# Optimization experiments

Hardware: AMD Instinct MI355X
Metric: run time of the kernel (lower is better)

## Reference

```python
import jax, jax.numpy as jnp
import numpy as np


def _conv(x, w, stride=1, pad=0):
    return jax.lax.conv_general_dilated(
        x, w, window_strides=(stride, stride),
        padding=[(pad, pad), (pad, pad)],
        dimension_numbers=('NCHW', 'OIHW', 'NCHW'))


def _frozen_bn(x, gamma, beta, mean, var):
    # FrozenBatchNorm2d: scale = gamma * rsqrt(var); bias = beta - mean*scale
    scale = gamma * jax.lax.rsqrt(var)
    bias = beta - mean * scale
    return x * scale[None, :, None, None] + bias[None, :, None, None]


def setup_inputs() -> dict:
    key = jax.random.key(0)
    ks = jax.random.split(key, 16)
    N, Cin, H, W = 32, 1024, 28, 28
    Cb, Cout = 256, 1024
    x = jax.random.normal(ks[0], (N, Cin, H, W), dtype=jnp.float32)
    # conv weights, kaiming-uniform-ish scale
    w1 = jax.random.uniform(ks[1], (Cb, Cin, 1, 1), minval=-1, maxval=1) * (1.0 / np.sqrt(Cin))
    w2 = jax.random.uniform(ks[2], (Cb, Cb, 3, 3), minval=-1, maxval=1) * (1.0 / np.sqrt(Cb * 9))
    w3 = jax.random.uniform(ks[3], (Cout, Cb, 1, 1), minval=-1, maxval=1) * (1.0 / np.sqrt(Cb))
    def bn_params(k, n):
        k1, k2, k3, k4 = jax.random.split(k, 4)
        gamma = jax.random.uniform(k1, (n,), minval=0.5, maxval=1.5)
        beta = jax.random.normal(k2, (n,)) * 0.1
        mean = jax.random.normal(k3, (n,)) * 0.1
        var = jax.random.uniform(k4, (n,), minval=0.5, maxval=1.5)
        return gamma, beta, mean, var
    g1, b1, m1, v1 = bn_params(ks[4], Cb)
    g2, b2, m2, v2 = bn_params(ks[5], Cb)
    g3, b3, m3, v3 = bn_params(ks[6], Cout)
    return dict(x=x, w1=w1, w2=w2, w3=w3,
                g1=g1, b1=b1, m1=m1, v1=v1,
                g2=g2, b2=b2, m2=m2, v2=v2,
                g3=g3, b3=b3, m3=m3, v3=v3)


def reference(x, w1, w2, w3, g1, b1, m1, v1, g2, b2, m2, v2, g3, b3, m3, v3):
    identity = x
    out = _conv(x, w1, stride=1, pad=0)          # 1x1: Cin -> Cb
    out = jax.nn.relu(_frozen_bn(out, g1, b1, m1, v1))
    out = _conv(out, w2, stride=1, pad=1)        # 3x3: Cb -> Cb
    out = jax.nn.relu(_frozen_bn(out, g2, b2, m2, v2))
    out = _conv(out, w3, stride=1, pad=0)        # 1x1: Cb -> Cout
    out = _frozen_bn(out, g3, b3, m3, v3)
    # stride==1 and in_channels==out_channels -> downsample is None
    out = jax.nn.relu(out + identity)
    return out
```

## Files before the change

### kernel.cpp

```cpp
#include <hip/hip_runtime.h>


#define BM 128
#define BNT 128
#define BK 64

typedef __attribute__((ext_vector_type(8))) short short8;
typedef __attribute__((ext_vector_type(4))) float f32x4;

__device__ inline unsigned short f2bf(float f) {
    unsigned int u = __float_as_uint(f);
    u += 0x7fff + ((u >> 16) & 1);
    return (unsigned short)(u >> 16);
}

__device__ inline void gload16(const unsigned short* g, unsigned short* l) {
    __builtin_amdgcn_global_load_lds(
        (const __attribute__((address_space(1))) unsigned int*)g,
        (__attribute__((address_space(3))) unsigned int*)l, 16, 0, 0);
}

__global__ __launch_bounds__(256) void prep_x(const float* __restrict__ x,
                                              unsigned short* __restrict__ Xh) {
    __shared__ float t[32][33];
    const int p0 = blockIdx.x * 32, c0 = blockIdx.y * 32, n = blockIdx.z;
    const int tid = threadIdx.x;
    const int pl = tid & 31, cl = tid >> 5;
    const float* xb = x + ((size_t)n * 1024 + c0) * 784;
    #pragma unroll
    for (int j = 0; j < 4; ++j) {
        int ci = cl + j * 8;
        int p = p0 + pl;
        t[ci][pl] = (p < 784) ? xb[(size_t)ci * 784 + p] : 0.f;
    }
    __syncthreads();
    const int c2 = (tid & 15) * 2, pr = tid >> 4;
    #pragma unroll
    for (int j = 0; j < 2; ++j) {
        int p = p0 + pr + j * 16;
        if (p < 784) {
            unsigned int pk = (unsigned)f2bf(t[c2][pr + j * 16]) |
                              ((unsigned)f2bf(t[c2 + 1][pr + j * 16]) << 16);
            *(unsigned int*)(Xh + (size_t)(n * 784 + p) * 1024 + c0 + c2) = pk;
        }
    }
}

__global__ __launch_bounds__(256) void prep_w(
    const float* __restrict__ w1, const float* __restrict__ w2, const float* __restrict__ w3,
    const float* g1, const float* b1, const float* m1, const float* v1,
    const float* g2, const float* b2, const float* m2, const float* v2,
    const float* g3, const float* b3, const float* m3, const float* v3,
    unsigned short* __restrict__ Wb1, unsigned short* __restrict__ Wt2,
    unsigned short* __restrict__ Wb3,
    float* __restrict__ bn1, float* __restrict__ bn2, float* __restrict__ bn3) {
    int i = blockIdx.x * 256 + threadIdx.x;
    if (i < 262144) Wb1[i] = f2bf(w1[i]);
    if (i < 589824) {
        int kw = i % 3, t1 = i / 3;
        int kh = t1 % 3, t2 = t1 / 3;
        int ci = t2 & 255, co = t2 >> 8;
        Wt2[(size_t)((kh * 3 + kw) * 256 + co) * 256 + ci] = f2bf(w2[i]);
    }
    if (i < 262144) Wb3[i] = f2bf(w3[i]);
    if (i < 256) { float s = g1[i] * rsqrtf(v1[i]); bn1[i] = s; bn1[256 + i] = b1[i] - m1[i] * s; }
    if (i < 256) { float s = g2[i] * rsqrtf(v2[i]); bn2[i] = s; bn2[256 + i] = b2[i] - m2[i] * s; }
    if (i < 1024) { float s = g3[i] * rsqrtf(v3[i]); bn3[i] = s; bn3[1024 + i] = b3[i] - m3[i] * s; }
}

__global__ __launch_bounds__(256) void zero16(uint4* __restrict__ p, int n) {
    int i = blockIdx.x * 256 + threadIdx.x;
    if (i < n) p[i] = make_uint4(0u, 0u, 0u, 0u);
}

template <int CX, int NTAPS, int LAYER>
__device__ __forceinline__ void conv_body(
    const unsigned short* __restrict__ Xg, const unsigned short* __restrict__ Wg,
    const float* __restrict__ bn, int nco,
    const float* __restrict__ residual,
    unsigned short* __restrict__ obf, float* __restrict__ ofp) {
    __shared__ __align__(16) char smem[LAYER == 3 ? 33792 : 32768];
    unsigned short* Xs = (unsigned short*)smem;
    unsigned short* Ws = (unsigned short*)(smem + 16384);
    const int tid = threadIdx.x;
    const int wave = tid >> 6, lane = tid & 63;
    const int quad = lane >> 4, l15 = lane & 15;
    const int Pb = blockIdx.x * BM;
    const int cb = blockIdx.y * BNT;
    const int wco = (wave & 1) * 64;
    const int wpx = (wave >> 1) * 64;

    int rowt[4], cso[4];
    size_t xrow[4];
    #pragma unroll
    for (int t = 0; t < 4; ++t) {
        int slot = t * 256 + tid;
        int row = slot >> 3;
        int c = slot & 7;
        rowt[t] = row;
        cso[t] = ((c ^ (row & 7)) * 8);
        if (LAYER == 2) {
            int P = Pb + row;
            int n = P / 784, rem = P - n * 784;
            int h = rem / 28, w = rem - h * 28;
            xrow[t] = (size_t)n * 900 + h * 30 + w;
        } else {
            xrow[t] = (size_t)(Pb + row);
        }
    }

    f32x4 acc[4][4];
    #pragma unroll
    for (int i = 0; i < 4; ++i)
        #pragma unroll
        for (int j = 0; j < 4; ++j)
            acc[i][j] = (f32x4){0.f, 0.f, 0.f, 0.f};

    for (int tap = 0; tap < NTAPS; ++tap) {
        const int tapofs = (NTAPS == 9) ? ((tap / 3) * 30 + (tap % 3)) : 0;
        const unsigned short* Wtap = Wg + (size_t)tap * 256 * CX;
        for (int k0 = 0; k0 < CX; k0 += BK) {
            __syncthreads();
            #pragma unroll
            for (int t = 0; t < 4; ++t) {
                unsigned short* xl = Xs + (size_t)(t * 256 + wave * 64) * 8;
                unsigned short* wl = Ws + (size_t)(t * 256 + wave * 64) * 8;
                const unsigned short* gx = Xg + (xrow[t] + tapofs) * (size_t)CX + k0 + cso[t];
                const unsigned short* gw = Wtap + (size_t)(cb + rowt[t]) * CX + k0 + cso[t];
                gload16(gx, xl);
                gload16(gw, wl);
            }
            __syncthreads();
            #pragma unroll
            for (int kk = 0; kk < BK; kk += 32) {
                short8 af[4], bf[4];
                const int cbase = kk >> 3;
                #pragma unroll
                for (int wi = 0; wi < 4; ++wi) {
                    int row = wco + wi * 16 + l15;
                    int ch = (cbase + quad) ^ (row & 7);
                    af[wi] = *(const short8*)(Ws + (row * 8 + ch) * 8);
                }
                #pragma unroll
                for (int wj = 0; wj < 4; ++wj) {
                    int row = wpx + wj * 16 + l15;
                    int ch = (cbase + quad) ^ (row & 7);
                    bf[wj] = *(const short8*)(Xs + (row * 8 + ch) * 8);
                }
                #pragma unroll
                for (int wi = 0; wi < 4; ++wi)
                    #pragma unroll
                    for (int wj = 0; wj < 4; ++wj)
                        acc[wi][wj] = __builtin_amdgcn_mfma_f32_16x16x32_bf16(
                            af[wi], bf[wj], acc[wi][wj], 0, 0, 0);
            }
        }
    }

    __syncthreads();

    if (LAYER == 3) {
        float* ep = (float*)smem;
        #pragma unroll
        for (int pass = 0; pass < 2; ++pass) {
            if ((wave & 1) == pass) {
                #pragma unroll
                for (int wi = 0; wi < 4; ++wi) {
                    int co0 = cb + wco + wi * 16 + quad * 4;
                    f32x4 sc = *(const f32x4*)(bn + co0);
                    f32x4 bi = *(const f32x4*)(bn + nco + co0);
                    int cr0 = wi * 16 + quad * 4;
                    #pragma unroll
                    for (int wj = 0; wj < 4; ++wj) {
                        int px = wpx + wj * 16 + l15;
                        #pragma unroll
                        for (int r = 0; r < 4; ++r)
                            ep[(cr0 + r) * 132 + px] = fmaf(acc[wi][wj][r], sc[r], bi[r]);
                    }
                }
            }
            __syncthreads();
            {
                int cr = tid >> 2;
                int cg = tid & 3;
                int co = cb + pass * 64 + cr;
                #pragma unroll
                for (int k = 0; k < 8; ++k) {
                    int px4 = (cg + 4 * k) * 4;
                    f32x4 v = *(const f32x4*)(ep + cr * 132 + px4);
                    int P = Pb + px4;
                    int n = P / 784, p = P - n * 784;
                    size_t off = ((size_t)n * 1024 + co) * 784 + p;
                    float4 rs = *(const float4*)(residual + off);
                    float4 o;
                    o.x = v[0] + rs.x; o.x = o.x > 0.f ? o.x : 0.f;
                    o.y = v[1] + rs.y; o.y = o.y > 0.f ? o.y : 0.f;
                    o.z = v[2] + rs.z; o.z = o.z > 0.f ? o.z : 0.f;
                    o.w = v[3] + rs.w; o.w = o.w > 0.f ? o.w : 0.f;
                    *(float4*)(ofp + off) = o;
                }
            }
            __syncthreads();
        }
    } else {
        unsigned short* ep = (unsigned short*)smem;
        #pragma unroll
        for (int pass = 0; pass < 2; ++pass) {
            if ((wave >> 1) == pass) {
                #pragma unroll
                for (int wi = 0; wi < 4; ++wi) {
                    int co0 = cb + wco + wi * 16 + quad * 4;
                    f32x4 sc = *(const f32x4*)(bn + co0);
                    f32x4 bi = *(const f32x4*)(bn + nco + co0);
                    int col = wco + wi * 16 + quad * 4;
                    #pragma unroll
                    for (int wj = 0; wj < 4; ++wj) {
                        int pxl = wj * 16 + l15;
                        float v0 = fmaf(acc[wi][wj][0], sc[0], bi[0]); v0 = v0 > 0.f ? v0 : 0.f;
                        float v1 = fmaf(acc[wi][wj][1], sc[1], bi[1]); v1 = v1 > 0.f ? v1 : 0.f;
                        float v2 = fmaf(acc[wi][wj][2], sc[2], bi[2]); v2 = v2 > 0.f ? v2 : 0.f;
                        float v3 = fmaf(acc[wi][wj][3], sc[3], bi[3]); v3 = v3 > 0.f ? v3 : 0.f;
                        uint2 pk;
                        pk.x = (unsigned)f2bf(v0) | ((unsigned)f2bf(v1) << 16);
                        pk.y = (unsigned)f2bf(v2) | ((unsigned)f2bf(v3) << 16);
                        *(uint2*)(ep + pxl * 136 + col) = pk;
                    }
                }
            }
            __syncthreads();
            {
                int pxl = tid >> 2;
                int cg = tid & 3;
                int P = Pb + pass * 64 + pxl;
                size_t orow;
                if (LAYER == 1) {
                    int n = P / 784, rem = P - n * 784;
                    int h = rem / 28, w = rem - h * 28;
                    orow = (size_t)n * 900 + (h + 1) * 30 + (w + 1);
                } else {
                    orow = (size_t)P;
                }
                #pragma unroll
                for (int k = 0; k < 4; ++k) {
                    int cc = (cg + 4 * k) * 8;
                    uint4 v = *(const uint4*)(ep + pxl * 136 + cc);
                    *(uint4*)(obf + orow * 256 + cb + cc) = v;
                }
            }
            __syncthreads();
        }
    }
}

__global__ __launch_bounds__(256) void conv1_mfma(
    const unsigned short* __restrict__ Xg, const unsigned short* __restrict__ Wg,
    const float* __restrict__ bn, unsigned short* __restrict__ obf) {
    conv_body<1024, 1, 1>(Xg, Wg, bn, 256, nullptr, obf, nullptr);
}
__global__ __launch_bounds__(256) void conv2_mfma(
    const unsigned short* __restrict__ Xg, const unsigned short* __restrict__ Wg,
    const float* __restrict__ bn, unsigned short* __restrict__ obf) {
    conv_body<256, 9, 2>(Xg, Wg, bn, 256, nullptr, obf, nullptr);
}
__global__ __launch_bounds__(256) void conv3_mfma(
    const unsigned short* __restrict__ Xg, const unsigned short* __restrict__ Wg,
    const float* __restrict__ bn, const float* __restrict__ residual,
    float* __restrict__ ofp) {
    conv_body<256, 1, 3>(Xg, Wg, bn, 1024, residual, nullptr, ofp);
}

extern "C" void kernel_launch(void* const* d_in, const int* in_sizes, int n_in,
                              void* d_out, int out_size, void* d_ws, size_t ws_size,
                              hipStream_t stream) {
    const float* x  = (const float*)d_in[0];
    const float* w1 = (const float*)d_in[1];
    const float* w2 = (const float*)d_in[2];
    const float* w3 = (const float*)d_in[3];
    const float* g1 = (const float*)d_in[4];  const float* b1 = (const float*)d_in[5];
    const float* m1 = (const float*)d_in[6];  const float* v1 = (const float*)d_in[7];
    const float* g2 = (const float*)d_in[8];  const float* b2 = (const float*)d_in[9];
    const float* m2 = (const float*)d_in[10]; const float* v2 = (const float*)d_in[11];
    const float* g3 = (const float*)d_in[12]; const float* b3 = (const float*)d_in[13];
    const float* m3 = (const float*)d_in[14]; const float* v3 = (const float*)d_in[15];
    float* out = (float*)d_out;

    char* ws = (char*)d_ws;
    unsigned short* Xh  = (unsigned short*)(ws);
    unsigned short* y1p = (unsigned short*)(ws + 51380224);
    unsigned short* y2  = (unsigned short*)(ws + 66125824);
    unsigned short* Wb1 = (unsigned short*)(ws + 78970880);
    unsigned short* Wt2 = (unsigned short*)(ws + 79495168);
    unsigned short* Wb3 = (unsigned short*)(ws + 80674816);
    float* bn1 = (float*)(ws + 81199104);
    float* bn2 = (float*)(ws + 81201152);
    float* bn3 = (float*)(ws + 81203200);

    prep_x<<<dim3(25, 32, 32), 256, 0, stream>>>(x, Xh);
    prep_w<<<2304, 256, 0, stream>>>(w1, w2, w3,
                                     g1, b1, m1, v1, g2, b2, m2, v2, g3, b3, m3, v3,
                                     Wb1, Wt2, Wb3, bn1, bn2, bn3);
    zero16<<<3600, 256, 0, stream>>>((uint4*)y1p, 921600);

    conv1_mfma<<<dim3(196, 2), 256, 0, stream>>>(Xh, Wb1, bn1, y1p);
    conv2_mfma<<<dim3(196, 2), 256, 0, stream>>>(y1p, Wt2, bn2, y2);
    conv3_mfma<<<dim3(196, 8), 256, 0, stream>>>(y2, Wb3, bn3, x, out);
}
```

Measured before the change: 343.2 us.

## Fuse fp32-to-bf16 input transpose into conv1 and zero only padding border

Drops the separate prep_x kernel, which transposed x from NCHW fp32 to NHWC bf16 in a workspace buffer. conv1 now reads fp32 x directly with float4 loads, converts to bf16, and writes the swizzled tile into LDS itself. The full zeroing of the padded y1 buffer is replaced by a kernel that writes only the 116 border cells per image. This saves a full read and write pass over x plus most of the zeroing traffic. In exchange, conv1 uses synchronous register-staged loads instead of direct global-to-LDS loads, which may expose more load latency.

```diff
diff --git a/kernel.cpp b/kernel.cpp
--- a/kernel.cpp
+++ b/kernel.cpp
@@ -18,32 +18,6 @@
     __builtin_amdgcn_global_load_lds(
         (const __attribute__((address_space(1))) unsigned int*)g,
         (__attribute__((address_space(3))) unsigned int*)l, 16, 0, 0);
-}
-
-__global__ __launch_bounds__(256) void prep_x(const float* __restrict__ x,
-                                              unsigned short* __restrict__ Xh) {
-    __shared__ float t[32][33];
-    const int p0 = blockIdx.x * 32, c0 = blockIdx.y * 32, n = blockIdx.z;
-    const int tid = threadIdx.x;
-    const int pl = tid & 31, cl = tid >> 5;
-    const float* xb = x + ((size_t)n * 1024 + c0) * 784;
-    #pragma unroll
-    for (int j = 0; j < 4; ++j) {
-        int ci = cl + j * 8;
-        int p = p0 + pl;
-        t[ci][pl] = (p < 784) ? xb[(size_t)ci * 784 + p] : 0.f;
-    }
-    __syncthreads();
-    const int c2 = (tid & 15) * 2, pr = tid >> 4;
-    #pragma unroll
-    for (int j = 0; j < 2; ++j) {
-        int p = p0 + pr + j * 16;
-        if (p < 784) {
-            unsigned int pk = (unsigned)f2bf(t[c2][pr + j * 16]) |
-                              ((unsigned)f2bf(t[c2 + 1][pr + j * 16]) << 16);
-            *(unsigned int*)(Xh + (size_t)(n * 784 + p) * 1024 + c0 + c2) = pk;
-        }
-    }
 }
 
 __global__ __launch_bounds__(256) void prep_w(
@@ -68,13 +42,23 @@
     if (i < 1024) { float s = g3[i] * rsqrtf(v3[i]); bn3[i] = s; bn3[1024 + i] = b3[i] - m3[i] * s; }
 }
 
-__global__ __launch_bounds__(256) void zero16(uint4* __restrict__ p, int n) {
+__global__ __launch_bounds__(256) void border_zero(uint4* __restrict__ y1p) {
     int i = blockIdx.x * 256 + threadIdx.x;
-    if (i < n) p[i] = make_uint4(0u, 0u, 0u, 0u);
+    int ch8 = i & 31;
+    int t = i >> 5;
+    int cell = t % 116;
+    int n = t / 116;
+    int h, w;
+    if (cell < 30)      { h = 0;          w = cell; }
+    else if (cell < 60) { h = 29;         w = cell - 30; }
+    else if (cell < 88) { h = cell - 59;  w = 0; }
+    else                { h = cell - 87;  w = 29; }
+    y1p[((size_t)n * 900 + h * 30 + w) * 32 + ch8] = make_uint4(0u, 0u, 0u, 0u);
 }
 
 template <int CX, int NTAPS, int LAYER>
 __device__ __forceinline__ void conv_body(
+    const float* __restrict__ Xf,
     const unsigned short* __restrict__ Xg, const unsigned short* __restrict__ Wg,
     const float* __restrict__ bn, int nco,
     const float* __restrict__ residual,
@@ -109,6 +93,20 @@
         }
     }
 
+    const int cp = tid & 31;
+    size_t xbase[4];
+    int plr[4];
+    if (LAYER == 1) {
+        #pragma unroll
+        for (int r = 0; r < 4; ++r) {
+            int pl = ((tid >> 5) + r * 8) * 4;
+            int P = Pb + pl;
+            int n = P / 784, p = P - n * 784;
+            plr[r] = pl;
+            xbase[r] = ((size_t)n * 1024 + 2 * cp) * 784 + p;
+        }
+    }
+
     f32x4 acc[4][4];
     #pragma unroll
     for (int i = 0; i < 4; ++i)
@@ -123,12 +121,31 @@
             __syncthreads();
             #pragma unroll
             for (int t = 0; t < 4; ++t) {
-                unsigned short* xl = Xs + (size_t)(t * 256 + wave * 64) * 8;
                 unsigned short* wl = Ws + (size_t)(t * 256 + wave * 64) * 8;
-                const unsigned short* gx = Xg + (xrow[t] + tapofs) * (size_t)CX + k0 + cso[t];
-                const unsigned short* gw = Wtap + (size_t)(cb + rowt[t]) * CX + k0 + cso[t];
-                gload16(gx, xl);
-                gload16(gw, wl);
+                gload16(Wtap + (size_t)(cb + rowt[t]) * CX + k0 + cso[t], wl);
+            }
+            if (LAYER == 1) {
+                #pragma unroll
+                for (int r = 0; r < 4; ++r) {
+                    const float* src = Xf + xbase[r] + (size_t)k0 * 784;
+                    float4 a = *(const float4*)src;
+                    float4 b = *(const float4*)(src + 784);
+                    float av[4] = {a.x, a.y, a.z, a.w};
+                    float bv[4] = {b.x, b.y, b.z, b.w};
+                    #pragma unroll
+                    for (int j = 0; j < 4; ++j) {
+                        unsigned u = (unsigned)f2bf(av[j]) | ((unsigned)f2bf(bv[j]) << 16);
+                        int row = plr[r] + j;
+                        int dw = row * 32 + (((cp >> 2) ^ (row & 7)) << 2) + (cp & 3);
+                        ((unsigned*)Xs)[dw] = u;
+                    }
+                }
+            } else {
+                #pragma unroll
+                for (int t = 0; t < 4; ++t) {
+                    unsigned short* xl = Xs + (size_t)(t * 256 + wave * 64) * 8;
+                    gload16(Xg + (xrow[t] + tapofs) * (size_t)CX + k0 + cso[t], xl);
+                }
             }
             __syncthreads();
             #pragma unroll
@@ -253,20 +270,20 @@
 }
 
 __global__ __launch_bounds__(256) void conv1_mfma(
-    const unsigned short* __restrict__ Xg, const unsigned short* __restrict__ Wg,
+    const float* __restrict__ Xf, const unsigned short* __restrict__ Wg,
     const float* __restrict__ bn, unsigned short* __restrict__ obf) {
-    conv_body<1024, 1, 1>(Xg, Wg, bn, 256, nullptr, obf, nullptr);
+    conv_body<1024, 1, 1>(Xf, nullptr, Wg, bn, 256, nullptr, obf, nullptr);
 }
 __global__ __launch_bounds__(256) void conv2_mfma(
     const unsigned short* __restrict__ Xg, const unsigned short* __restrict__ Wg,
     const float* __restrict__ bn, unsigned short* __restrict__ obf) {
-    conv_body<256, 9, 2>(Xg, Wg, bn, 256, nullptr, obf, nullptr);
+    conv_body<256, 9, 2>(nullptr, Xg, Wg, bn, 256, nullptr, obf, nullptr);
 }
 __global__ __launch_bounds__(256) void conv3_mfma(
     const unsigned short* __restrict__ Xg, const unsigned short* __restrict__ Wg,
     const float* __restrict__ bn, const float* __restrict__ residual,
     float* __restrict__ ofp) {
-    conv_body<256, 1, 3>(Xg, Wg, bn, 1024, residual, nullptr, ofp);
+    conv_body<256, 1, 3>(nullptr, Xg, Wg, bn, 1024, residual, nullptr, ofp);
 }
 
 extern "C" void kernel_launch(void* const* d_in, const int* in_sizes, int n_in,
@@ -285,23 +302,21 @@
     float* out = (float*)d_out;
 
     char* ws = (char*)d_ws;
-    unsigned short* Xh  = (unsigned short*)(ws);
-    unsigned short* y1p = (unsigned short*)(ws + 51380224);
-    unsigned short* y2  = (unsigned short*)(ws + 66125824);
-    unsigned short* Wb1 = (unsigned short*)(ws + 78970880);
-    unsigned short* Wt2 = (unsigned short*)(ws + 79495168);
-    unsigned short* Wb3 = (unsigned short*)(ws + 80674816);
-    float* bn1 = (float*)(ws + 81199104);
-    float* bn2 = (float*)(ws + 81201152);
-    float* bn3 = (float*)(ws + 81203200);
-
-    prep_x<<<dim3(25, 32, 32), 256, 0, stream>>>(x, Xh);
+    unsigned short* y1p = (unsigned short*)(ws);
+    unsigned short* y2  = (unsigned short*)(ws + 14745600);
+    unsigned short* Wb1 = (unsigned short*)(ws + 27590656);
+    unsigned short* Wt2 = (unsigned short*)(ws + 28114944);
+    unsigned short* Wb3 = (unsigned short*)(ws + 29294592);
+    float* bn1 = (float*)(ws + 29818880);
+    float* bn2 = (float*)(ws + 29820928);
+    float* bn3 = (float*)(ws + 29822976);
+
     prep_w<<<2304, 256, 0, stream>>>(w1, w2, w3,
                                      g1, b1, m1, v1, g2, b2, m2, v2, g3, b3, m3, v3,
                                      Wb1, Wt2, Wb3, bn1, bn2, bn3);
-    zero16<<<3600, 256, 0, stream>>>((uint4*)y1p, 921600);
-
-    conv1_mfma<<<dim3(196, 2), 256, 0, stream>>>(Xh, Wb1, bn1, y1p);
+    border_zero<<<464, 256, 0, stream>>>((uint4*)y1p);
+
+    conv1_mfma<<<dim3(196, 2), 256, 0, stream>>>(x, Wb1, bn1, y1p);
     conv2_mfma<<<dim3(196, 2), 256, 0, stream>>>(y1p, Wt2, bn2, y2);
     conv3_mfma<<<dim3(196, 8), 256, 0, stream>>>(y2, Wb3, bn3, x, out);
 }
```

Result: faster. 325.0 us (-5.3%).
